# Kernel tuning notes

Measured on AMD Instinct MI355X. Metric: run time of the kernel, lower is better.

## Reference

```python
import jax, jax.numpy as jnp
import numpy as np

B, N, DIM = 32, 1024, 768
H, S, D = 16, 4, 64  # num_heads, num_subheads (L=H*S=64), attn_dim


def setup_inputs() -> dict:
    key = jax.random.key(0)
    k1, k2, k3, k4 = jax.random.split(key, 4)
    x = jax.random.normal(k1, (B, N, DIM), dtype=jnp.float32)
    eos_indices = jax.random.randint(k2, (B,), 0, N)
    # q_emb: original shape (1,H,S,1,D); singleton dims dropped -> (H,S,D)
    q_emb = jax.random.normal(k3, (H, S, D), dtype=jnp.float32)
    # k Linear(dim -> H*D), xavier-uniform weight, zero bias (share_kv: v == k)
    limit = float(np.sqrt(6.0 / (DIM + H * D)))
    Wk = jax.random.uniform(k4, (DIM, H * D), dtype=jnp.float32, minval=-limit, maxval=limit)
    bk = jnp.zeros((H * D,), dtype=jnp.float32)
    return {"x": x, "eos_indices": eos_indices, "q_emb": q_emb, "Wk": Wk, "bk": bk}


def reference(x, eos_indices, q_emb, Wk, bk):
    # x: (B,N,dim); shared k/v projection -> (B,N,H,D)
    kv = (x @ Wk + bk).reshape(x.shape[0], x.shape[1], H, D)
    scale = D ** -0.5
    # Avoid the torch expand over subheads: contract directly.
    # logits: (B,H,S,N)
    logits = jnp.einsum("hsd,bnhd->bhsn", q_emb * scale, kv)
    # eos masking: positions strictly after eos index are masked out
    mask = jnp.arange(x.shape[1])[None, None, None, :] > eos_indices[:, None, None, None]
    logits = jnp.where(mask, -jnp.inf, logits)
    attn = jax.nn.softmax(logits, axis=-1)
    # weighted sum over N -> (B,H,S,D) -> (B,L,D)
    out = jnp.einsum("bhsn,bnhd->bhsd", attn, kv)
    return out.reshape(x.shape[0], H * S, D)
```

## Files before the change

kernel.cpp:

```cpp
#include <hip/hip_runtime.h>
#include <hip/hip_bf16.h>
#include <stdint.h>

typedef float  f32x4  __attribute__((ext_vector_type(4)));
typedef __bf16 bf16x4 __attribute__((ext_vector_type(4)));
typedef __bf16 bf16x8 __attribute__((ext_vector_type(8)));
typedef unsigned int u32x2 __attribute__((ext_vector_type(2)));
typedef unsigned int u32x4 __attribute__((ext_vector_type(4)));

#define AS1 __attribute__((address_space(1)))
#define AS3 __attribute__((address_space(3)))

__device__ __forceinline__ void async_load16(const void* g, void* lds) {
    __builtin_amdgcn_global_load_lds((const AS1 unsigned int*)g,
                                     (AS3 unsigned int*)lds, 16, 0, 0);
}

__global__ __launch_bounds__(256) void qw_kernel(const float* __restrict__ q_emb,
                                                 const float* __restrict__ wk,
                                                 __bf16* __restrict__ qwT) {
    __shared__ float qlds[256];
    __shared__ float part[4096];
    const int t = threadIdx.x;
    const int kc = blockIdx.x;
    const int h  = blockIdx.y;
    const int k0 = kc * 64;
    qlds[t] = q_emb[h * 256 + t] * 0.125f;
    __syncthreads();
    const int dseg = t & 15;
    const int krow = t >> 4;
#pragma unroll
    for (int i = 0; i < 4; ++i) {
        const int k = i * 16 + krow;
        f32x4 wv = *(const f32x4*)&wk[(size_t)(k0 + k) * 1024 + h * 64 + dseg * 4];
#pragma unroll
        for (int s = 0; s < 4; ++s) {
            float p = qlds[s * 64 + dseg * 4 + 0] * wv[0]
                    + qlds[s * 64 + dseg * 4 + 1] * wv[1]
                    + qlds[s * 64 + dseg * 4 + 2] * wv[2]
                    + qlds[s * 64 + dseg * 4 + 3] * wv[3];
            part[k * 64 + s * 16 + dseg] = p;
        }
    }
    __syncthreads();
    const int k = t >> 2, s = t & 3;
    const float* pp = &part[k * 64 + s * 16];
    float sum = 0.f;
#pragma unroll
    for (int j = 0; j < 16; ++j) sum += pp[j];
    qwT[(h * 4 + s) * 768 + k0 + k] = (__bf16)sum;
}

__global__ __launch_bounds__(512, 4) void logits_kernel(const float* __restrict__ x,
                                                        const __bf16* __restrict__ qwT,
                                                        const int* __restrict__ eos_idx,
                                                        float* __restrict__ Lg,
                                                        float* __restrict__ partials) {
    __shared__ char smem[32768];
    char* Bl = smem;
    char* Al = smem + 16384;
    const int t = threadIdx.x, l = t & 63, w = t >> 6;
    const int m0 = blockIdx.x * 64;
    const int bb = m0 >> 10, n0 = m0 & 1023;
    const int chunk = (m0 >> 6) & 15;
    const int wm = (w >> 1) * 16;
    const int wh = (w & 1) * 32;

    f32x4 acc[2];
    acc[0] = (f32x4)0.f; acc[1] = (f32x4)0.f;

    const int Bcol = t >> 3, Bseg = t & 7;
    const __bf16* qsrc = qwT + Bcol * 768 + (Bseg ^ (Bcol & 7)) * 8;
    const int Arow = t >> 3;
    const float* xrow = &x[(size_t)(m0 + Arow) * 768 + (t & 7) * 8];
    const int Adst = (Arow * 128 + (t & 7) * 16) ^ ((Arow & 7) << 4);

    f32x4 av0, av1;
    async_load16(qsrc, Bl + t * 16);
    av0 = *(const f32x4*)(xrow);
    av1 = *(const f32x4*)(xrow + 4);
    {
        bf16x8 v;
        v[0] = (__bf16)av0[0]; v[1] = (__bf16)av0[1];
        v[2] = (__bf16)av0[2]; v[3] = (__bf16)av0[3];
        v[4] = (__bf16)av1[0]; v[5] = (__bf16)av1[1];
        v[6] = (__bf16)av1[2]; v[7] = (__bf16)av1[3];
        *(bf16x8*)(Al + Adst) = v;
    }
    asm volatile("s_waitcnt vmcnt(0)" ::: "memory");
    __syncthreads();

    int buf = 0;
    for (int step = 0; step < 12; ++step) {
        const int nbuf = buf ^ 1;
        const bool more = (step + 1) < 12;
        if (more) {
            const int kt = (step + 1) * 64;
            async_load16(qsrc + kt, Bl + nbuf * 8192 + t * 16);
            av0 = *(const f32x4*)(xrow + kt);
            av1 = *(const f32x4*)(xrow + kt + 4);
        }
#pragma unroll
        for (int kh = 0; kh < 2; ++kh) {
            const int u = kh * 4 + (l >> 4);
            const int arow = wm + (l & 15);
            bf16x8 af = *(const bf16x8*)(Al + buf * 8192 +
                                         ((arow * 128 + u * 16) ^ ((arow & 7) << 4)));
            bf16x8 bfr[2];
#pragma unroll
            for (int j = 0; j < 2; ++j) {
                const int col = wh + j * 16 + (l & 15);
                bfr[j] = *(const bf16x8*)(Bl + buf * 8192 +
                                          ((col * 128 + u * 16) ^ ((col & 7) << 4)));
            }
#pragma unroll
            for (int j = 0; j < 2; ++j)
                acc[j] = __builtin_amdgcn_mfma_f32_16x16x32_bf16(af, bfr[j], acc[j], 0, 0, 0);
        }
        if (more) {
            bf16x8 v;
            v[0] = (__bf16)av0[0]; v[1] = (__bf16)av0[1];
            v[2] = (__bf16)av0[2]; v[3] = (__bf16)av0[3];
            v[4] = (__bf16)av1[0]; v[5] = (__bf16)av1[1];
            v[6] = (__bf16)av1[2]; v[7] = (__bf16)av1[3];
            *(bf16x8*)(Al + nbuf * 8192 + Adst) = v;
        }
        asm volatile("s_waitcnt vmcnt(0)" ::: "memory");
        __syncthreads();
        buf = nbuf;
    }

#pragma unroll
    for (int j = 0; j < 2; ++j) {
        const int hs = wh + j * 16 + (l & 15);
        const int nb = wm + (l >> 4) * 4;
        *(f32x4*)(smem + ((hs * 256 + nb * 4) ^ ((hs & 7) << 4))) = acc[j];
    }
    __syncthreads();
    const int eosb = eos_idx[bb];
    const int hs = t >> 3, seg = t & 7;
    const int fH = (hs & 7) << 4;
    f32x4 v0 = *(const f32x4*)(smem + ((hs * 256 + seg * 32) ^ fH));
    f32x4 v1 = *(const f32x4*)(smem + ((hs * 256 + seg * 32 + 16) ^ fH));
    const int nbase = n0 + seg * 8;
    float mx = -INFINITY;
#pragma unroll
    for (int j = 0; j < 4; ++j) {
        if (nbase + j > eosb) v0[j] = -INFINITY;
        if (nbase + 4 + j > eosb) v1[j] = -INFINITY;
        mx = fmaxf(mx, fmaxf(v0[j], v1[j]));
    }
    *(f32x4*)&Lg[(size_t)bb * 65536 + hs * 1024 + nbase] = v0;
    *(f32x4*)&Lg[(size_t)bb * 65536 + hs * 1024 + nbase + 4] = v1;
#pragma unroll
    for (int off = 1; off < 8; off <<= 1) mx = fmaxf(mx, __shfl_xor(mx, off));
    float sl = 0.f;
    if (mx > -INFINITY) {
#pragma unroll
        for (int j = 0; j < 4; ++j) sl += __expf(v0[j] - mx) + __expf(v1[j] - mx);
    }
#pragma unroll
    for (int off = 1; off < 8; off <<= 1) sl += __shfl_xor(sl, off);
    if (seg == 0) {
        float2 st = {mx, sl};
        *(float2*)&partials[(size_t)(((bb * 16 + chunk) * 64) + hs) * 2] = st;
    }
}

__global__ __launch_bounds__(256, 3) void pv_kernel(const float* __restrict__ x,
                                                    const float* __restrict__ Lg,
                                                    const float* __restrict__ partials,
                                                    float* __restrict__ y) {
    __shared__ char smem[32768];
    char* Pl = smem;
    char* Xl = smem + 16384;
    const int t = threadIdx.x, l = t & 63, w = t >> 6;
    const int vid = (blockIdx.x & 7) * 96 + (blockIdx.x >> 3);
    const int b = vid / 24, rem = vid % 24;
    const int kc = rem % 12, nh = rem / 12;
    const int k0 = kc * 64, nbase = nh * 512;
    const int wrA = (w >> 1) * 32, wcB = (w & 1) * 32;
    const float* Lgb = Lg + (size_t)b * 65536;
    const float* xb = x + (size_t)b * 786432 + k0 + l;
    const int fK = ((l & 7) << 4) | (((l >> 3) & 1) << 3);

    const int r0 = t >> 3, r1 = 32 + (t >> 3);
    float m0r, i0r, m1r, i1r;
    {
        const float* pb = partials + (size_t)b * 2048;
        float m = -INFINITY, m2 = -INFINITY;
#pragma unroll
        for (int c = 0; c < 16; ++c) {
            m  = fmaxf(m,  pb[(c * 64 + r0) * 2]);
            m2 = fmaxf(m2, pb[(c * 64 + r1) * 2]);
        }
        float s = 0.f, s2 = 0.f;
#pragma unroll
        for (int c = 0; c < 16; ++c) {
            float2 p0 = *(const float2*)&pb[(c * 64 + r0) * 2];
            float2 p1 = *(const float2*)&pb[(c * 64 + r1) * 2];
            s  += p0.y * __expf(p0.x - m);
            s2 += p1.y * __expf(p1.x - m2);
        }
        m0r = m; i0r = 1.0f / s;
        m1r = m2; i1r = 1.0f / s2;
    }
    const int n0s0 = (((t & 7) ^ (r0 & 7)) * 8);
    const int n0s1 = (((t & 7) ^ (r1 & 7)) * 8);

    f32x4 acc[2][2];
#pragma unroll
    for (int i = 0; i < 2; ++i)
#pragma unroll
        for (int j = 0; j < 2; ++j) acc[i][j] = (f32x4)0.f;

    float xv[16];
    f32x4 plo0, phi0, plo1, phi1;

    plo0 = *(const f32x4*)&Lgb[(size_t)r0 * 1024 + nbase + n0s0];
    phi0 = *(const f32x4*)&Lgb[(size_t)r0 * 1024 + nbase + n0s0 + 4];
    plo1 = *(const f32x4*)&Lgb[(size_t)r1 * 1024 + nbase + n0s1];
    phi1 = *(const f32x4*)&Lgb[(size_t)r1 * 1024 + nbase + n0s1 + 4];
#pragma unroll
    for (int i = 0; i < 4; ++i)
#pragma unroll
        for (int j = 0; j < 4; ++j)
            xv[i * 4 + j] = xb[(size_t)(nbase + i * 16 + w * 4 + j) * 768];
    {
        bf16x8 pk;
#pragma unroll
        for (int j = 0; j < 4; ++j) pk[j]     = (__bf16)(__expf(plo0[j] - m0r) * i0r);
#pragma unroll
        for (int j = 0; j < 4; ++j) pk[4 + j] = (__bf16)(__expf(phi0[j] - m0r) * i0r);
        *(bf16x8*)(Pl + t * 16) = pk;
#pragma unroll
        for (int j = 0; j < 4; ++j) pk[j]     = (__bf16)(__expf(plo1[j] - m1r) * i1r);
#pragma unroll
        for (int j = 0; j < 4; ++j) pk[4 + j] = (__bf16)(__expf(phi1[j] - m1r) * i1r);
        *(bf16x8*)(Pl + 4096 + t * 16) = pk;
#pragma unroll
        for (int i = 0; i < 4; ++i) {
            bf16x4 vv = {(__bf16)xv[i * 4 + 0], (__bf16)xv[i * 4 + 1],
                         (__bf16)xv[i * 4 + 2], (__bf16)xv[i * 4 + 3]};
            *(bf16x4*)(Xl + ((l * 128 + (i * 16 + w * 4) * 2) ^ fK)) = vv;
        }
    }
    __syncthreads();

    int buf = 0;
    for (int step = 0; step < 8; ++step) {
        const int nbuf = buf ^ 1;
        const bool more = (step + 1) < 8;
        if (more) {
            const int nt = nbase + (step + 1) * 64;
            plo0 = *(const f32x4*)&Lgb[(size_t)r0 * 1024 + nt + n0s0];
            phi0 = *(const f32x4*)&Lgb[(size_t)r0 * 1024 + nt + n0s0 + 4];
            plo1 = *(const f32x4*)&Lgb[(size_t)r1 * 1024 + nt + n0s1];
            phi1 = *(const f32x4*)&Lgb[(size_t)r1 * 1024 + nt + n0s1 + 4];
#pragma unroll
            for (int i = 0; i < 4; ++i)
#pragma unroll
                for (int j = 0; j < 4; ++j)
                    xv[i * 4 + j] = xb[(size_t)(nt + i * 16 + w * 4 + j) * 768];
        }
#pragma unroll
        for (int kh = 0; kh < 2; ++kh) {
            const int u = kh * 4 + (l >> 4);
            bf16x8 af[2], bfr[2];
#pragma unroll
            for (int i = 0; i < 2; ++i) {
                const int row = wrA + i * 16 + (l & 15);
                af[i] = *(const bf16x8*)(Pl + buf * 8192 +
                                         ((row * 128 + u * 16) ^ ((row & 7) << 4)));
            }
#pragma unroll
            for (int j = 0; j < 2; ++j) {
                const int kcol = wcB + j * 16 + (l & 15);
                const int fKc = ((kcol & 7) << 4) | (((kcol >> 3) & 1) << 3);
                const int addrA = kcol * 128 + kh * 64 + (l >> 4) * 16;
                u32x2 lo = *(const u32x2*)(Xl + buf * 8192 + (addrA ^ fKc));
                u32x2 hi = *(const u32x2*)(Xl + buf * 8192 + ((addrA + 8) ^ fKc));
                u32x4 uu = {lo[0], lo[1], hi[0], hi[1]};
                bfr[j] = __builtin_bit_cast(bf16x8, uu);
            }
#pragma unroll
            for (int i = 0; i < 2; ++i)
#pragma unroll
                for (int j = 0; j < 2; ++j)
                    acc[i][j] = __builtin_amdgcn_mfma_f32_16x16x32_bf16(
                        af[i], bfr[j], acc[i][j], 0, 0, 0);
        }
        if (more) {
            bf16x8 pk;
#pragma unroll
            for (int j = 0; j < 4; ++j) pk[j]     = (__bf16)(__expf(plo0[j] - m0r) * i0r);
#pragma unroll
            for (int j = 0; j < 4; ++j) pk[4 + j] = (__bf16)(__expf(phi0[j] - m0r) * i0r);
            *(bf16x8*)(Pl + nbuf * 8192 + t * 16) = pk;
#pragma unroll
            for (int j = 0; j < 4; ++j) pk[j]     = (__bf16)(__expf(plo1[j] - m1r) * i1r);
#pragma unroll
            for (int j = 0; j < 4; ++j) pk[4 + j] = (__bf16)(__expf(phi1[j] - m1r) * i1r);
            *(bf16x8*)(Pl + nbuf * 8192 + 4096 + t * 16) = pk;
#pragma unroll
            for (int i = 0; i < 4; ++i) {
                bf16x4 vv = {(__bf16)xv[i * 4 + 0], (__bf16)xv[i * 4 + 1],
                             (__bf16)xv[i * 4 + 2], (__bf16)xv[i * 4 + 3]};
                *(bf16x4*)(Xl + nbuf * 8192 + ((l * 128 + (i * 16 + w * 4) * 2) ^ fK)) = vv;
            }
        }
        __syncthreads();
        buf = nbuf;
    }

#pragma unroll
    for (int i = 0; i < 2; ++i)
#pragma unroll
        for (int j = 0; j < 2; ++j) {
            const int kcol = wcB + j * 16 + (l & 15);
#pragma unroll
            for (int r = 0; r < 4; ++r) {
                const int hs2 = wrA + i * 16 + (l >> 4) * 4 + r;
                *(float*)(smem + ((hs2 * 256 + kcol * 4) ^ ((hs2 & 7) << 4))) = acc[i][j][r];
            }
        }
    __syncthreads();
    float* yh = y + (size_t)nh * 1572864;
    const int hs2 = t >> 2;
#pragma unroll
    for (int i = 0; i < 4; ++i) {
        const int seg = (t & 3) + i * 4;
        f32x4 v = *(const f32x4*)(smem + ((hs2 * 256 + seg * 16) ^ ((hs2 & 7) << 4)));
        *(f32x4*)&yh[(size_t)(b * 64 + hs2) * 768 + k0 + seg * 4] = v;
    }
}

__global__ __launch_bounds__(256) void out_kernel(const float* __restrict__ y,
                                                  const float* __restrict__ wk,
                                                  const float* __restrict__ bk,
                                                  float* __restrict__ out) {
    __shared__ float ylds[8 * 768];
    __shared__ float red[2048];
    const int t = threadIdx.x;
    const int vid = (blockIdx.x & 7) * 32 + (blockIdx.x >> 3);
    const int h = vid >> 4, bp = vid & 15;
#pragma unroll
    for (int r = 0; r < 8; ++r) {
        const int gb = bp * 2 + (r >> 2);
        const int hs = h * 4 + (r & 3);
#pragma unroll
        for (int i = 0; i < 3; ++i) {
            const size_t idx = (size_t)(gb * 64 + hs) * 768 + i * 256 + t;
            ylds[r * 768 + i * 256 + t] = y[idx] + y[idx + 1572864];
        }
    }
    __syncthreads();
    const int kp = t >> 6, d = t & 63;
    float acc[8] = {0.f, 0.f, 0.f, 0.f, 0.f, 0.f, 0.f, 0.f};
    for (int i = 0; i < 48; ++i) {
        const int k = kp * 192 + i * 4;
        const float wv0 = wk[(size_t)(k + 0) * 1024 + h * 64 + d];
        const float wv1 = wk[(size_t)(k + 1) * 1024 + h * 64 + d];
        const float wv2 = wk[(size_t)(k + 2) * 1024 + h * 64 + d];
        const float wv3 = wk[(size_t)(k + 3) * 1024 + h * 64 + d];
#pragma unroll
        for (int r = 0; r < 8; ++r) {
            f32x4 yv = *(const f32x4*)&ylds[r * 768 + k];
            acc[r] += yv[0] * wv0 + yv[1] * wv1 + yv[2] * wv2 + yv[3] * wv3;
        }
    }
#pragma unroll
    for (int r = 0; r < 8; ++r) red[(r * 64 + d) * 4 + kp] = acc[r];
    __syncthreads();
#pragma unroll
    for (int i = 0; i < 2; ++i) {
        const int o = i * 256 + t;
        const int r = o >> 6, dd = o & 63;
        f32x4 pv = *(const f32x4*)&red[o * 4];
        const float s = pv[0] + pv[1] + pv[2] + pv[3] + bk[h * 64 + dd];
        const int gb = bp * 2 + (r >> 2);
        out[(size_t)(gb * 64 + h * 4 + (r & 3)) * 64 + dd] = s;
    }
}

extern "C" void kernel_launch(void* const* d_in, const int* in_sizes, int n_in,
                              void* d_out, int out_size, void* d_ws, size_t ws_size,
                              hipStream_t stream) {
    const float* x     = (const float*)d_in[0];
    const int*   eos   = (const int*)d_in[1];
    const float* q_emb = (const float*)d_in[2];
    const float* Wk    = (const float*)d_in[3];
    const float* bk    = (const float*)d_in[4];
    float* out = (float*)d_out;

    char* ws = (char*)d_ws;
    __bf16* qwT      = (__bf16*)ws;
    float*  Lg       = (float*)(ws + 131072);
    float*  partials = (float*)(ws + 8519680);
    float*  y        = (float*)(ws + 8781824);

    qw_kernel<<<dim3(12, 16), 256, 0, stream>>>(q_emb, Wk, qwT);
    logits_kernel<<<dim3(512), 512, 0, stream>>>(x, qwT, eos, Lg, partials);
    pv_kernel<<<dim3(768), 256, 0, stream>>>(x, Lg, partials, y);
    out_kernel<<<dim3(256), 256, 0, stream>>>(y, Wk, bk, out);
}
```

Before: 65.10 us.

## Deepen global-load prefetch in logits and PV kernels with register rotation

The logits kernel now keeps x tiles three steps ahead in rotating register sets, using explicit vmcnt waits and raw s_barrier so B-tile async loads can stay in flight across iterations. The PV kernel double-buffers its register prefetch (A/B sets) so the global loads for step t+2 are issued before computing step t. The goal is to hide global memory latency behind MFMA work. The cost is higher register pressure, which may reduce occupancy, and fragile hand-written wait counts.

```diff
diff --git a/kernel.cpp b/kernel.cpp
--- a/kernel.cpp
+++ b/kernel.cpp
@@ -49,6 +49,24 @@
 #pragma unroll
     for (int j = 0; j < 16; ++j) sum += pp[j];
     qwT[(h * 4 + s) * 768 + k0 + k] = (__bf16)sum;
+}
+
+__device__ __forceinline__ void lg_compute(const char* Al, const char* Bl, int buf,
+                                           int wm, int wh, int l, f32x4* acc) {
+#pragma unroll
+    for (int kh = 0; kh < 2; ++kh) {
+        const int u = kh * 4 + (l >> 4);
+        const int arow = wm + (l & 15);
+        bf16x8 af = *(const bf16x8*)(Al + buf * 8192 +
+                                     ((arow * 128 + u * 16) ^ ((arow & 7) << 4)));
+#pragma unroll
+        for (int j = 0; j < 2; ++j) {
+            const int col = wh + j * 16 + (l & 15);
+            bf16x8 bfr = *(const bf16x8*)(Bl + buf * 8192 +
+                                          ((col * 128 + u * 16) ^ ((col & 7) << 4)));
+            acc[j] = __builtin_amdgcn_mfma_f32_16x16x32_bf16(af, bfr, acc[j], 0, 0, 0);
+        }
+    }
 }
 
 __global__ __launch_bounds__(512, 4) void logits_kernel(const float* __restrict__ x,
@@ -75,60 +93,69 @@
     const float* xrow = &x[(size_t)(m0 + Arow) * 768 + (t & 7) * 8];
     const int Adst = (Arow * 128 + (t & 7) * 16) ^ ((Arow & 7) << 4);
 
-    f32x4 av0, av1;
-    async_load16(qsrc, Bl + t * 16);
-    av0 = *(const f32x4*)(xrow);
-    av1 = *(const f32x4*)(xrow + 4);
+    f32x4 xa0, xa1, xb0, xb1, xc0, xc1;
+
+#define LG_ISSUE_B(T, BUF) async_load16(qsrc + (T) * 64, Bl + (BUF) * 8192 + t * 16)
+#define LG_ISSUE_X(R0, R1, T) { R0 = *(const f32x4*)(xrow + (T) * 64); \
+                                R1 = *(const f32x4*)(xrow + (T) * 64 + 4); }
+#define LG_WRITE_X(R0, R1, BUF) { bf16x8 v_; \
+    v_[0]=(__bf16)R0[0]; v_[1]=(__bf16)R0[1]; v_[2]=(__bf16)R0[2]; v_[3]=(__bf16)R0[3]; \
+    v_[4]=(__bf16)R1[0]; v_[5]=(__bf16)R1[1]; v_[6]=(__bf16)R1[2]; v_[7]=(__bf16)R1[3]; \
+    *(bf16x8*)(Al + (BUF) * 8192 + Adst) = v_; }
+
+    LG_ISSUE_B(0, 0);
+    __builtin_amdgcn_sched_barrier(0);
+    LG_ISSUE_X(xa0, xa1, 0);
+    LG_ISSUE_X(xb0, xb1, 1);
+    LG_ISSUE_X(xc0, xc1, 2);
+    LG_WRITE_X(xa0, xa1, 0);
+    asm volatile("s_waitcnt lgkmcnt(0)" ::: "memory");
+    asm volatile("s_waitcnt vmcnt(4)" ::: "memory");
+    __builtin_amdgcn_s_barrier();
+
+    int buf = 0;
+#define LG_STEP(T, W0, W1, I0, I1) { \
+    const int nbuf = buf ^ 1; \
+    LG_ISSUE_B((T) + 1, nbuf); \
+    __builtin_amdgcn_sched_barrier(0); \
+    LG_ISSUE_X(I0, I1, (T) + 3); \
+    lg_compute(Al, Bl, buf, wm, wh, l, acc); \
+    LG_WRITE_X(W0, W1, nbuf); \
+    asm volatile("s_waitcnt lgkmcnt(0)" ::: "memory"); \
+    asm volatile("s_waitcnt vmcnt(2)" ::: "memory"); \
+    __builtin_amdgcn_s_barrier(); \
+    buf = nbuf; }
+
+    for (int it = 0; it < 3; ++it) {
+        const int tb = it * 3;
+        LG_STEP(tb + 0, xb0, xb1, xa0, xa1);
+        LG_STEP(tb + 1, xc0, xc1, xb0, xb1);
+        LG_STEP(tb + 2, xa0, xa1, xc0, xc1);
+    }
     {
-        bf16x8 v;
-        v[0] = (__bf16)av0[0]; v[1] = (__bf16)av0[1];
-        v[2] = (__bf16)av0[2]; v[3] = (__bf16)av0[3];
-        v[4] = (__bf16)av1[0]; v[5] = (__bf16)av1[1];
-        v[6] = (__bf16)av1[2]; v[7] = (__bf16)av1[3];
-        *(bf16x8*)(Al + Adst) = v;
-    }
-    asm volatile("s_waitcnt vmcnt(0)" ::: "memory");
-    __syncthreads();
-
-    int buf = 0;
-    for (int step = 0; step < 12; ++step) {
         const int nbuf = buf ^ 1;
-        const bool more = (step + 1) < 12;
-        if (more) {
-            const int kt = (step + 1) * 64;
-            async_load16(qsrc + kt, Bl + nbuf * 8192 + t * 16);
-            av0 = *(const f32x4*)(xrow + kt);
-            av1 = *(const f32x4*)(xrow + kt + 4);
-        }
-#pragma unroll
-        for (int kh = 0; kh < 2; ++kh) {
-            const int u = kh * 4 + (l >> 4);
-            const int arow = wm + (l & 15);
-            bf16x8 af = *(const bf16x8*)(Al + buf * 8192 +
-                                         ((arow * 128 + u * 16) ^ ((arow & 7) << 4)));
-            bf16x8 bfr[2];
-#pragma unroll
-            for (int j = 0; j < 2; ++j) {
-                const int col = wh + j * 16 + (l & 15);
-                bfr[j] = *(const bf16x8*)(Bl + buf * 8192 +
-                                          ((col * 128 + u * 16) ^ ((col & 7) << 4)));
-            }
-#pragma unroll
-            for (int j = 0; j < 2; ++j)
-                acc[j] = __builtin_amdgcn_mfma_f32_16x16x32_bf16(af, bfr[j], acc[j], 0, 0, 0);
-        }
-        if (more) {
-            bf16x8 v;
-            v[0] = (__bf16)av0[0]; v[1] = (__bf16)av0[1];
-            v[2] = (__bf16)av0[2]; v[3] = (__bf16)av0[3];
-            v[4] = (__bf16)av1[0]; v[5] = (__bf16)av1[1];
-            v[6] = (__bf16)av1[2]; v[7] = (__bf16)av1[3];
-            *(bf16x8*)(Al + nbuf * 8192 + Adst) = v;
-        }
+        LG_ISSUE_B(10, nbuf);
+        __builtin_amdgcn_sched_barrier(0);
+        lg_compute(Al, Bl, buf, wm, wh, l, acc);
+        LG_WRITE_X(xb0, xb1, nbuf);
+        asm volatile("s_waitcnt lgkmcnt(0)" ::: "memory");
         asm volatile("s_waitcnt vmcnt(0)" ::: "memory");
-        __syncthreads();
+        __builtin_amdgcn_s_barrier();
         buf = nbuf;
     }
+    {
+        const int nbuf = buf ^ 1;
+        LG_ISSUE_B(11, nbuf);
+        __builtin_amdgcn_sched_barrier(0);
+        lg_compute(Al, Bl, buf, wm, wh, l, acc);
+        LG_WRITE_X(xc0, xc1, nbuf);
+        asm volatile("s_waitcnt lgkmcnt(0)" ::: "memory");
+        asm volatile("s_waitcnt vmcnt(0)" ::: "memory");
+        __builtin_amdgcn_s_barrier();
+        buf = nbuf;
+    }
+    lg_compute(Al, Bl, buf, wm, wh, l, acc);
+    __syncthreads();
 
 #pragma unroll
     for (int j = 0; j < 2; ++j) {
@@ -164,6 +191,37 @@
     if (seg == 0) {
         float2 st = {mx, sl};
         *(float2*)&partials[(size_t)(((bb * 16 + chunk) * 64) + hs) * 2] = st;
+    }
+}
+
+__device__ __forceinline__ void pv_compute(const char* Pl, const char* Xl, int buf,
+                                           int wrA, int wcB, int l, f32x4 (*acc)[2]) {
+#pragma unroll
+    for (int kh = 0; kh < 2; ++kh) {
+        const int u = kh * 4 + (l >> 4);
+        bf16x8 af[2], bfr[2];
+#pragma unroll
+        for (int i = 0; i < 2; ++i) {
+            const int row = wrA + i * 16 + (l & 15);
+            af[i] = *(const bf16x8*)(Pl + buf * 8192 +
+                                     ((row * 128 + u * 16) ^ ((row & 7) << 4)));
+        }
+#pragma unroll
+        for (int j = 0; j < 2; ++j) {
+            const int kcol = wcB + j * 16 + (l & 15);
+            const int fKc = ((kcol & 7) << 4) | (((kcol >> 3) & 1) << 3);
+            const int addrA = kcol * 128 + kh * 64 + (l >> 4) * 16;
+            u32x2 lo = *(const u32x2*)(Xl + buf * 8192 + (addrA ^ fKc));
+            u32x2 hi = *(const u32x2*)(Xl + buf * 8192 + ((addrA + 8) ^ fKc));
+            u32x4 uu = {lo[0], lo[1], hi[0], hi[1]};
+            bfr[j] = __builtin_bit_cast(bf16x8, uu);
+        }
+#pragma unroll
+        for (int i = 0; i < 2; ++i)
+#pragma unroll
+            for (int j = 0; j < 2; ++j)
+                acc[i][j] = __builtin_amdgcn_mfma_f32_16x16x32_bf16(
+                    af[i], bfr[j], acc[i][j], 0, 0, 0);
     }
 }
 
@@ -214,104 +272,67 @@
 #pragma unroll
         for (int j = 0; j < 2; ++j) acc[i][j] = (f32x4)0.f;
 
-    float xv[16];
-    f32x4 plo0, phi0, plo1, phi1;
-
-    plo0 = *(const f32x4*)&Lgb[(size_t)r0 * 1024 + nbase + n0s0];
-    phi0 = *(const f32x4*)&Lgb[(size_t)r0 * 1024 + nbase + n0s0 + 4];
-    plo1 = *(const f32x4*)&Lgb[(size_t)r1 * 1024 + nbase + n0s1];
-    phi1 = *(const f32x4*)&Lgb[(size_t)r1 * 1024 + nbase + n0s1 + 4];
-#pragma unroll
-    for (int i = 0; i < 4; ++i)
-#pragma unroll
-        for (int j = 0; j < 4; ++j)
-            xv[i * 4 + j] = xb[(size_t)(nbase + i * 16 + w * 4 + j) * 768];
-    {
-        bf16x8 pk;
-#pragma unroll
-        for (int j = 0; j < 4; ++j) pk[j]     = (__bf16)(__expf(plo0[j] - m0r) * i0r);
-#pragma unroll
-        for (int j = 0; j < 4; ++j) pk[4 + j] = (__bf16)(__expf(phi0[j] - m0r) * i0r);
-        *(bf16x8*)(Pl + t * 16) = pk;
-#pragma unroll
-        for (int j = 0; j < 4; ++j) pk[j]     = (__bf16)(__expf(plo1[j] - m1r) * i1r);
-#pragma unroll
-        for (int j = 0; j < 4; ++j) pk[4 + j] = (__bf16)(__expf(phi1[j] - m1r) * i1r);
-        *(bf16x8*)(Pl + 4096 + t * 16) = pk;
-#pragma unroll
-        for (int i = 0; i < 4; ++i) {
-            bf16x4 vv = {(__bf16)xv[i * 4 + 0], (__bf16)xv[i * 4 + 1],
-                         (__bf16)xv[i * 4 + 2], (__bf16)xv[i * 4 + 3]};
-            *(bf16x4*)(Xl + ((l * 128 + (i * 16 + w * 4) * 2) ^ fK)) = vv;
-        }
-    }
-    __syncthreads();
+    f32x4 pAl0, pAh0, pAl1, pAh1, pBl0, pBh0, pBl1, pBh1;
+    float xvA[16], xvB[16];
+
+#define PV_ISSUE(PL0, PH0, PL1, PH1, XV, T) { \
+    const int nt_ = nbase + (T) * 64; \
+    PL0 = *(const f32x4*)&Lgb[(size_t)r0 * 1024 + nt_ + n0s0]; \
+    PH0 = *(const f32x4*)&Lgb[(size_t)r0 * 1024 + nt_ + n0s0 + 4]; \
+    PL1 = *(const f32x4*)&Lgb[(size_t)r1 * 1024 + nt_ + n0s1]; \
+    PH1 = *(const f32x4*)&Lgb[(size_t)r1 * 1024 + nt_ + n0s1 + 4]; \
+    _Pragma("unroll") \
+    for (int i_ = 0; i_ < 4; ++i_) { \
+        _Pragma("unroll") \
+        for (int j_ = 0; j_ < 4; ++j_) \
+            XV[i_ * 4 + j_] = xb[(size_t)(nt_ + i_ * 16 + w * 4 + j_) * 768]; } }
+
+#define PV_PACK(PL0, PH0, PL1, PH1, XV, BUF) { \
+    bf16x8 pk_; \
+    _Pragma("unroll") \
+    for (int j_ = 0; j_ < 4; ++j_) pk_[j_]     = (__bf16)(__expf(PL0[j_] - m0r) * i0r); \
+    _Pragma("unroll") \
+    for (int j_ = 0; j_ < 4; ++j_) pk_[4 + j_] = (__bf16)(__expf(PH0[j_] - m0r) * i0r); \
+    *(bf16x8*)(Pl + (BUF) * 8192 + t * 16) = pk_; \
+    _Pragma("unroll") \
+    for (int j_ = 0; j_ < 4; ++j_) pk_[j_]     = (__bf16)(__expf(PL1[j_] - m1r) * i1r); \
+    _Pragma("unroll") \
+    for (int j_ = 0; j_ < 4; ++j_) pk_[4 + j_] = (__bf16)(__expf(PH1[j_] - m1r) * i1r); \
+    *(bf16x8*)(Pl + (BUF) * 8192 + 4096 + t * 16) = pk_; \
+    _Pragma("unroll") \
+    for (int i_ = 0; i_ < 4; ++i_) { \
+        bf16x4 vv_ = {(__bf16)XV[i_ * 4 + 0], (__bf16)XV[i_ * 4 + 1], \
+                      (__bf16)XV[i_ * 4 + 2], (__bf16)XV[i_ * 4 + 3]}; \
+        *(bf16x4*)(Xl + (BUF) * 8192 + ((l * 128 + (i_ * 16 + w * 4) * 2) ^ fK)) = vv_; } }
+
+    PV_ISSUE(pAl0, pAh0, pAl1, pAh1, xvA, 0);
+    PV_ISSUE(pBl0, pBh0, pBl1, pBh1, xvB, 1);
+    PV_PACK(pAl0, pAh0, pAl1, pAh1, xvA, 0);
+    asm volatile("s_waitcnt lgkmcnt(0)" ::: "memory");
+    __builtin_amdgcn_s_barrier();
 
     int buf = 0;
-    for (int step = 0; step < 8; ++step) {
-        const int nbuf = buf ^ 1;
-        const bool more = (step + 1) < 8;
-        if (more) {
-            const int nt = nbase + (step + 1) * 64;
-            plo0 = *(const f32x4*)&Lgb[(size_t)r0 * 1024 + nt + n0s0];
-            phi0 = *(const f32x4*)&Lgb[(size_t)r0 * 1024 + nt + n0s0 + 4];
-            plo1 = *(const f32x4*)&Lgb[(size_t)r1 * 1024 + nt + n0s1];
-            phi1 = *(const f32x4*)&Lgb[(size_t)r1 * 1024 + nt + n0s1 + 4];
-#pragma unroll
-            for (int i = 0; i < 4; ++i)
-#pragma unroll
-                for (int j = 0; j < 4; ++j)
-                    xv[i * 4 + j] = xb[(size_t)(nt + i * 16 + w * 4 + j) * 768];
-        }
-#pragma unroll
-        for (int kh = 0; kh < 2; ++kh) {
-            const int u = kh * 4 + (l >> 4);
-            bf16x8 af[2], bfr[2];
-#pragma unroll
-            for (int i = 0; i < 2; ++i) {
-                const int row = wrA + i * 16 + (l & 15);
-                af[i] = *(const bf16x8*)(Pl + buf * 8192 +
-                                         ((row * 128 + u * 16) ^ ((row & 7) << 4)));
-            }
-#pragma unroll
-            for (int j = 0; j < 2; ++j) {
-                const int kcol = wcB + j * 16 + (l & 15);
-                const int fKc = ((kcol & 7) << 4) | (((kcol >> 3) & 1) << 3);
-                const int addrA = kcol * 128 + kh * 64 + (l >> 4) * 16;
-                u32x2 lo = *(const u32x2*)(Xl + buf * 8192 + (addrA ^ fKc));
-                u32x2 hi = *(const u32x2*)(Xl + buf * 8192 + ((addrA + 8) ^ fKc));
-                u32x4 uu = {lo[0], lo[1], hi[0], hi[1]};
-                bfr[j] = __builtin_bit_cast(bf16x8, uu);
-            }
-#pragma unroll
-            for (int i = 0; i < 2; ++i)
-#pragma unroll
-                for (int j = 0; j < 2; ++j)
-                    acc[i][j] = __builtin_amdgcn_mfma_f32_16x16x32_bf16(
-                        af[i], bfr[j], acc[i][j], 0, 0, 0);
-        }
-        if (more) {
-            bf16x8 pk;
-#pragma unroll
-            for (int j = 0; j < 4; ++j) pk[j]     = (__bf16)(__expf(plo0[j] - m0r) * i0r);
-#pragma unroll
-            for (int j = 0; j < 4; ++j) pk[4 + j] = (__bf16)(__expf(phi0[j] - m0r) * i0r);
-            *(bf16x8*)(Pl + nbuf * 8192 + t * 16) = pk;
-#pragma unroll
-            for (int j = 0; j < 4; ++j) pk[j]     = (__bf16)(__expf(plo1[j] - m1r) * i1r);
-#pragma unroll
-            for (int j = 0; j < 4; ++j) pk[4 + j] = (__bf16)(__expf(phi1[j] - m1r) * i1r);
-            *(bf16x8*)(Pl + nbuf * 8192 + 4096 + t * 16) = pk;
-#pragma unroll
-            for (int i = 0; i < 4; ++i) {
-                bf16x4 vv = {(__bf16)xv[i * 4 + 0], (__bf16)xv[i * 4 + 1],
-                             (__bf16)xv[i * 4 + 2], (__bf16)xv[i * 4 + 3]};
-                *(bf16x4*)(Xl + nbuf * 8192 + ((l * 128 + (i * 16 + w * 4) * 2) ^ fK)) = vv;
-            }
-        }
-        __syncthreads();
-        buf = nbuf;
-    }
+    for (int it = 0; it < 4; ++it) {
+        const int te = it * 2;
+        if (te + 2 < 8) PV_ISSUE(pAl0, pAh0, pAl1, pAh1, xvA, te + 2);
+        pv_compute(Pl, Xl, buf, wrA, wcB, l, acc);
+        if (te + 1 < 8) {
+            PV_PACK(pBl0, pBh0, pBl1, pBh1, xvB, buf ^ 1);
+            asm volatile("s_waitcnt lgkmcnt(0)" ::: "memory");
+            __builtin_amdgcn_s_barrier();
+        }
+        buf ^= 1;
+        const int to = te + 1;
+        if (to + 2 < 8) PV_ISSUE(pBl0, pBh0, pBl1, pBh1, xvB, to + 2);
+        pv_compute(Pl, Xl, buf, wrA, wcB, l, acc);
+        if (to + 1 < 8) {
+            PV_PACK(pAl0, pAh0, pAl1, pAh1, xvA, buf ^ 1);
+            asm volatile("s_waitcnt lgkmcnt(0)" ::: "memory");
+            __builtin_amdgcn_s_barrier();
+        }
+        buf ^= 1;
+    }
+    __syncthreads();
 
 #pragma unroll
     for (int i = 0; i < 2; ++i)
```

Measured after the change: 63.89 us. About the same (-1.9%).
